# Optimization experiments

Measured on AMD Instinct MI355X. Metric: run time of the kernel, lower is better.

## Reference

```python
import jax, jax.numpy as jnp
import numpy as np

N_POINTS = 65536      # total nodes across the batch
NDIMS = 3
NUM_THETAS = 64       # directions
BUMP_STEPS = 32       # discretization steps of [-radius, radius]
NUM_GRAPHS = 64       # number of point clouds in the batch
RADIUS = 1.1
SCALE = 100.0         # sigmoid sharpness


def setup_inputs() -> dict:
    key = jax.random.key(0)
    k1, k2, k3 = jax.random.split(key, 3)
    x = jax.random.normal(k1, (N_POINTS, NDIMS), dtype=jnp.float32)
    # unit-norm direction vectors on the sphere, columns of v: [ndims, num_thetas]
    v = jax.random.normal(k2, (NDIMS, NUM_THETAS), dtype=jnp.float32)
    v = v / jnp.linalg.norm(v, axis=0, keepdims=True)
    # lin = discretization of [-radius, radius], matches nn.Parameter linspace
    lin = jnp.linspace(-RADIUS, RADIUS, BUMP_STEPS, dtype=jnp.float32)
    # sorted batch index assigning each node to a graph (torch_geometric convention)
    batch = jnp.sort(jax.random.randint(k3, (N_POINTS,), 0, NUM_GRAPHS, dtype=jnp.int32))
    return {"x": x, "v": v, "lin": lin, "batch": batch}


def reference(x, v, lin, batch):
    # node heights: inner product of coordinates with each direction -> [N, T]
    nh = x @ v
    # broadcast soft-threshold: sigmoid(scale * (lin - nh)) -> [N, S, T]
    # (torch builds [S,1,N,T] then movedims to [N,1,S,T]; same values)
    ecc = jax.nn.sigmoid(SCALE * (lin[None, :, None] - nh[:, None, :]))
    # segment scatter-add over nodes per graph -> [B, S, T]
    ect = jax.ops.segment_sum(ecc, batch, num_segments=NUM_GRAPHS)
    return ect  # torch output after .squeeze(): [batch, bump_steps, num_thetas]
```

## Files before the change

### kernel.cpp

```cpp
#include <hip/hip_runtime.h>

#define T      64
#define S      32
#define NGRAPH 64
#define NSPLIT 8
#define NW     4

__global__ __launch_bounds__(256, 2) void ect_partial(
    const float* __restrict__ x, const float* __restrict__ v,
    const float* __restrict__ lin, const int* __restrict__ batch,
    float* __restrict__ ws, int n_points)
{
    __shared__ float bins[34 * 256];

    const int tid  = threadIdx.x;
    const int t    = tid & 63;
    const int w    = tid >> 6;
    const int b    = blockIdx.x;
    const int g    = b >> 3;
    const int c    = b & (NSPLIT - 1);

    {
        const float4 z4 = {0.0f, 0.0f, 0.0f, 0.0f};
        float4* b4 = (float4*)bins;
        for (int i = tid; i < 34 * 256 / 4; i += 256) b4[i] = z4;
    }

    const int target = (t < 32) ? g : (g + 1);
    const int i32    = t & 31;
    int lo = 0;
    const int strides[3] = {2048, 64, 2};
#pragma unroll
    for (int rnd = 0; rnd < 3; rnd++) {
        const int stride = strides[rnd];
        const int idx  = lo + i32 * stride;
        const int pv   = batch[min(idx, n_points - 1)];
        const bool prd = (idx < n_points) && (pv < target);
        const unsigned long long bal = __ballot(prd);
        const int cnt = __popc((unsigned)(bal >> (t & 32)));
        lo += max(cnt - 1, 0) * stride;
    }
    if ((lo < n_points) && (batch[min(lo, n_points - 1)] < target)) lo++;
    const int gstart = __builtin_amdgcn_readfirstlane(lo);
    const int gend   = __builtin_amdgcn_readlane(lo, 32);
    const int len    = gend - gstart;
    const int n0     = gstart + (len * c) / NSPLIT;
    const int n1     = gstart + (len * (c + 1)) / NSPLIT;

    const float lin0     = lin[0];
    const float step     = lin[1] - lin0;
    const float inv_step = 1.0f / step;
    const float nl0i     = -lin0 * inv_step;
    const float K2 = (100.0f * step) * 1.4426950408889634f;
    const float r  = __builtin_amdgcn_exp2f(-K2);

    const float v0 = v[0 * T + t];
    const float v1 = v[1 * T + t];
    const float v2 = v[2 * T + t];

    float v0acc = 0.0f;
    __syncthreads();

#pragma unroll 2
    for (int n = n0 + w; n < n1; n += NW) {
        const float x0 = x[3 * n + 0];
        const float x1 = x[3 * n + 1];
        const float x2 = x[3 * n + 2];
        const float nh = fmaf(x0, v0, fmaf(x1, v1, x2 * v2));
        const float f  = fmaf(nh, inv_step, nl0i);
        const float fs = ceilf(f);
        const int   ss = (int)fs;
        const float e0 = __builtin_amdgcn_exp2f(fmaf(K2, f - fs, K2));
        const float e1 = e0 * r;
        const float sm  = __builtin_amdgcn_rcpf(1.0f + e0);
        const float s0v = __builtin_amdgcn_rcpf(1.0f + e1);
        v0acc += (ss <= -1) ? 1.0f : (ss == 0 ? s0v : (ss == 1 ? sm : 0.0f));
        const int p0 = ss - 1, p1 = ss, p2 = ss + 1;
        const int a0 = (((unsigned)(p0 - 1) < 31u) ? p0 : 33) * 256 + tid;
        const int a1 = (((unsigned)(p1 - 1) < 31u) ? p1 : 33) * 256 + tid;
        const int a2 = (((unsigned)(p2 - 1) < 31u) ? p2 : 33) * 256 + tid;
        const float r0 = bins[a0], r1 = bins[a1], r2 = bins[a2];
        bins[a0] = r0 + sm;
        bins[a1] = r1 + (s0v - sm);
        bins[a2] = r2 + (1.0f - s0v);
    }

    bins[0 * 256 + tid] = v0acc;
    __syncthreads();

    for (int cell = tid; cell < 32 * 64; cell += 256) {
        const int cc = cell >> 6;
        const int tt = cell & 63;
        const float sum = bins[cc * 256 +   0 + tt] + bins[cc * 256 +  64 + tt]
                        + bins[cc * 256 + 128 + tt] + bins[cc * 256 + 192 + tt];
        bins[cc * 256 + tt] = sum;
    }
    __syncthreads();

    float run = bins[0 * 256 + t];
    const int sbase = 8 * w;
    for (int cc = 1; cc < sbase; cc++) run += bins[cc * 256 + t];
    float* wsb = ws + (size_t)b * (S * T);
#pragma unroll
    for (int j = 0; j < 8; j++) {
        const int s = sbase + j;
        if (s >= 1) run += bins[s * 256 + t];
        wsb[s * T + t] = run;
    }
}

__global__ __launch_bounds__(256) void ect_reduce(
    const float4* __restrict__ ws4, float4* __restrict__ out4)
{
    const int idx = blockIdx.x * 256 + threadIdx.x;
    const int g   = idx >> 9;
    const int i   = idx & 511;
    float4 sum = {0.0f, 0.0f, 0.0f, 0.0f};
#pragma unroll
    for (int c = 0; c < NSPLIT; c++) {
        const float4 a = ws4[(size_t)(g * NSPLIT + c) * 512 + i];
        sum.x += a.x; sum.y += a.y; sum.z += a.z; sum.w += a.w;
    }
    out4[idx] = sum;
}

extern "C" void kernel_launch(void* const* d_in, const int* in_sizes, int n_in,
                              void* d_out, int out_size, void* d_ws, size_t ws_size,
                              hipStream_t stream) {
    const float* x     = (const float*)d_in[0];
    const float* v     = (const float*)d_in[1];
    const float* lin   = (const float*)d_in[2];
    const int*   batch = (const int*)d_in[3];
    float* out = (float*)d_out;
    float* ws  = (float*)d_ws;

    const int n_points = in_sizes[0] / 3;

    ect_partial<<<NGRAPH * NSPLIT, 256, 0, stream>>>(x, v, lin, batch, ws, n_points);
    ect_reduce<<<NGRAPH * S * T / 4 / 256, 256, 0, stream>>>(
        (const float4*)ws, (float4*)out);
}
```

Before: 73.85 us.

## Split graphs across more blocks, contiguous per-wave chunks with batched x loads

Doubles the per-graph split from 8 to 16 blocks and raises occupancy to 4 blocks per CU by shrinking the LDS histogram from 34 to 32 rows. Out-of-range bin writes now go into row 0, which is overwritten by v0acc afterwards. Each wave now takes a contiguous slice of points and preloads 20 points' coordinates into registers per iteration, so global loads are issued in bulk. The reduce kernel is changed to float2 and sums 16 partials, which doubles the workspace traffic. The unrolled 60-float register buffer raises register pressure.

```diff
diff --git a/kernel.cpp b/kernel.cpp
--- a/kernel.cpp
+++ b/kernel.cpp
@@ -3,27 +3,29 @@
 #define T      64
 #define S      32
 #define NGRAPH 64
-#define NSPLIT 8
+#define NSPLIT 16
 #define NW     4
+#define MAXC   20
 
-__global__ __launch_bounds__(256, 2) void ect_partial(
+__global__ __launch_bounds__(256, 4) void ect_partial(
     const float* __restrict__ x, const float* __restrict__ v,
     const float* __restrict__ lin, const int* __restrict__ batch,
     float* __restrict__ ws, int n_points)
 {
-    __shared__ float bins[34 * 256];
+    __shared__ float bins[32 * 256];
 
     const int tid  = threadIdx.x;
     const int t    = tid & 63;
-    const int w    = tid >> 6;
+    const int w    = __builtin_amdgcn_readfirstlane(tid >> 6);
     const int b    = blockIdx.x;
-    const int g    = b >> 3;
+    const int g    = b >> 4;
     const int c    = b & (NSPLIT - 1);
 
     {
         const float4 z4 = {0.0f, 0.0f, 0.0f, 0.0f};
         float4* b4 = (float4*)bins;
-        for (int i = tid; i < 34 * 256 / 4; i += 256) b4[i] = z4;
+#pragma unroll
+        for (int i = 0; i < 8; i++) b4[tid + i * 256] = z4;
     }
 
     const int target = (t < 32) ? g : (g + 1);
@@ -47,6 +49,10 @@
     const int n0     = gstart + (len * c) / NSPLIT;
     const int n1     = gstart + (len * (c + 1)) / NSPLIT;
 
+    const int len_s = n1 - n0;
+    int       nw0   = n0 + (len_s * w) / NW;
+    const int nw1   = n0 + (len_s * (w + 1)) / NW;
+
     const float lin0     = lin[0];
     const float step     = lin[1] - lin0;
     const float inv_step = 1.0f / step;
@@ -61,31 +67,47 @@
     float v0acc = 0.0f;
     __syncthreads();
 
-#pragma unroll 2
-    for (int n = n0 + w; n < n1; n += NW) {
-        const float x0 = x[3 * n + 0];
-        const float x1 = x[3 * n + 1];
-        const float x2 = x[3 * n + 2];
-        const float nh = fmaf(x0, v0, fmaf(x1, v1, x2 * v2));
-        const float f  = fmaf(nh, inv_step, nl0i);
-        const float fs = ceilf(f);
-        const int   ss = (int)fs;
-        const float e0 = __builtin_amdgcn_exp2f(fmaf(K2, f - fs, K2));
-        const float e1 = e0 * r;
-        const float sm  = __builtin_amdgcn_rcpf(1.0f + e0);
-        const float s0v = __builtin_amdgcn_rcpf(1.0f + e1);
-        v0acc += (ss <= -1) ? 1.0f : (ss == 0 ? s0v : (ss == 1 ? sm : 0.0f));
-        const int p0 = ss - 1, p1 = ss, p2 = ss + 1;
-        const int a0 = (((unsigned)(p0 - 1) < 31u) ? p0 : 33) * 256 + tid;
-        const int a1 = (((unsigned)(p1 - 1) < 31u) ? p1 : 33) * 256 + tid;
-        const int a2 = (((unsigned)(p2 - 1) < 31u) ? p2 : 33) * 256 + tid;
-        const float r0 = bins[a0], r1 = bins[a1], r2 = bins[a2];
-        bins[a0] = r0 + sm;
-        bins[a1] = r1 + (s0v - sm);
-        bins[a2] = r2 + (1.0f - s0v);
+    const int xlim = 3 * n_points;
+
+    while (nw0 < nw1) {
+        const int cnt = min(nw1 - nw0, MAXC);
+        const int b3  = 3 * nw0;
+        float xs[3 * MAXC];
+        if (b3 + 3 * MAXC <= xlim) {
+#pragma unroll
+            for (int i = 0; i < 3 * MAXC; i++) xs[i] = x[b3 + i];
+        } else {
+#pragma unroll
+            for (int i = 0; i < 3 * MAXC; i++) xs[i] = x[min(b3 + i, xlim - 1)];
+        }
+#pragma unroll
+        for (int k = 0; k < MAXC; k++) {
+            const float x0 = xs[3 * k + 0];
+            const float x1 = xs[3 * k + 1];
+            const float x2 = xs[3 * k + 2];
+            const float nh = fmaf(x0, v0, fmaf(x1, v1, x2 * v2));
+            const float f  = fmaf(nh, inv_step, nl0i);
+            const float fs = ceilf(f);
+            const int   sr = (int)fs;
+            const int   ss = (k < cnt) ? sr : 64;
+            const float e0 = __builtin_amdgcn_exp2f(fmaf(K2, f - fs, K2));
+            const float e1 = e0 * r;
+            const float sm  = __builtin_amdgcn_rcpf(1.0f + e0);
+            const float s0v = __builtin_amdgcn_rcpf(1.0f + e1);
+            v0acc += (ss <= -1) ? 1.0f : (ss == 0 ? s0v : (ss == 1 ? sm : 0.0f));
+            const int p0 = ss - 1, p1 = ss, p2 = ss + 1;
+            const int a0 = (((unsigned)(p0 - 1) < 31u) ? p0 : 0) * 256 + tid;
+            const int a1 = (((unsigned)(p1 - 1) < 31u) ? p1 : 0) * 256 + tid;
+            const int a2 = (((unsigned)(p2 - 1) < 31u) ? p2 : 0) * 256 + tid;
+            const float r0 = bins[a0], r1 = bins[a1], r2 = bins[a2];
+            bins[a0] = r0 + sm;
+            bins[a1] = r1 + (s0v - sm);
+            bins[a2] = r2 + (1.0f - s0v);
+        }
+        nw0 += MAXC;
     }
 
-    bins[0 * 256 + tid] = v0acc;
+    bins[tid] = v0acc;
     __syncthreads();
 
     for (int cell = tid; cell < 32 * 64; cell += 256) {
@@ -110,18 +132,18 @@
 }
 
 __global__ __launch_bounds__(256) void ect_reduce(
-    const float4* __restrict__ ws4, float4* __restrict__ out4)
+    const float2* __restrict__ ws2, float2* __restrict__ out2)
 {
     const int idx = blockIdx.x * 256 + threadIdx.x;
-    const int g   = idx >> 9;
-    const int i   = idx & 511;
-    float4 sum = {0.0f, 0.0f, 0.0f, 0.0f};
+    const int g   = idx >> 10;
+    const int i   = idx & 1023;
+    float2 sum = {0.0f, 0.0f};
 #pragma unroll
     for (int c = 0; c < NSPLIT; c++) {
-        const float4 a = ws4[(size_t)(g * NSPLIT + c) * 512 + i];
-        sum.x += a.x; sum.y += a.y; sum.z += a.z; sum.w += a.w;
+        const float2 a = ws2[(size_t)(g * NSPLIT + c) * 1024 + i];
+        sum.x += a.x; sum.y += a.y;
     }
-    out4[idx] = sum;
+    out2[idx] = sum;
 }
 
 extern "C" void kernel_launch(void* const* d_in, const int* in_sizes, int n_in,
@@ -137,6 +159,6 @@
     const int n_points = in_sizes[0] / 3;
 
     ect_partial<<<NGRAPH * NSPLIT, 256, 0, stream>>>(x, v, lin, batch, ws, n_points);
-    ect_reduce<<<NGRAPH * S * T / 4 / 256, 256, 0, stream>>>(
-        (const float4*)ws, (float4*)out);
+    ect_reduce<<<NGRAPH * S * T / 2 / 256, 256, 0, stream>>>(
+        (const float2*)ws, (float2*)out);
 }
```

Measured after the change: 74.00 us. No clear change (+0.2%).
